# Kernel tuning notes

Hardware: AMD Instinct MI355X
Metric: run time of the kernel (lower is better)

## Reference

```python
import jax, jax.numpy as jnp
import numpy as np

IN_FEATURES = 512
OUT_FEATURES = 512
GRID_MIN = -2.0
GRID_MAX = 2.0
NUM_GRIDS = 8
SPLINE_SCALE = 0.1
BATCH = 16384


def setup_inputs() -> dict:
    key = jax.random.key(0)
    kx, kw = jax.random.split(key)
    x = jax.random.normal(kx, (BATCH, IN_FEATURES), dtype=jnp.float32)
    grid = jnp.linspace(GRID_MIN, GRID_MAX, NUM_GRIDS, dtype=jnp.float32)
    spline_weight = (
        jax.random.normal(kw, (IN_FEATURES * NUM_GRIDS, OUT_FEATURES), dtype=jnp.float32)
        * SPLINE_SCALE
    )
    return {"x": x, "grid": grid, "spline_weight": spline_weight}


def reference(x, grid, spline_weight):
    # denominator h = (grid_max - grid_min) / (num_grids - 1)
    h = (GRID_MAX - GRID_MIN) / (NUM_GRIDS - 1)
    # basis: [B, in_features, num_grids]
    basis = jnp.exp(-jnp.square((x[..., None] - grid) / h))
    # flatten to [B, in_features * num_grids] and GEMM
    return basis.reshape(basis.shape[0], -1) @ spline_weight
```

## Files before the change

### kernel.cpp

```cpp
#include <hip/hip_runtime.h>
#include <hip/hip_bf16.h>

#define BATCH 16384
#define IN_F 512
#define OUT_F 512
#define NG 8
#define KTOT (IN_F * NG)

#define SH    2.1019642153762872f
#define SSTEP 1.2011224087864498f
#define BC0N  4.2039284307525745f
#define RC1   2.4022448175728996f
#define RC2  -1.4426950408889634f
#define RQ    0.13533528323661270f

typedef __attribute__((ext_vector_type(8))) short short8;
typedef __attribute__((ext_vector_type(4))) float f32x4;
typedef __attribute__((ext_vector_type(2))) float f32x2;
typedef __attribute__((ext_vector_type(4))) unsigned int u32x4;
typedef __attribute__((ext_vector_type(2))) unsigned int u32x2;

__device__ __forceinline__ unsigned fbits(float f) {
    union { float f; unsigned u; } v; v.f = f; return v.u;
}
__device__ __forceinline__ unsigned pack2bf(float lo, float hi) {
    unsigned a = (fbits(lo) + 0x8000u) >> 16;
    unsigned b = (fbits(hi) + 0x8000u) & 0xFFFF0000u;
    return a | b;
}

__device__ __forceinline__ void lds_barrier() {
    __asm__ volatile("" ::: "memory");
    __builtin_amdgcn_sched_barrier(0);
    __builtin_amdgcn_s_waitcnt(0xC07F);
    __builtin_amdgcn_s_barrier();
    __builtin_amdgcn_sched_barrier(0);
    __asm__ volatile("" ::: "memory");
}

__global__ void wt_swizzle(const float* __restrict__ W, unsigned short* __restrict__ Wt) {
    const int gid  = blockIdx.x * 256 + threadIdx.x;
    const int lane = gid & 63;
    const int f    = (gid >> 6) & 7;
    const int kt   = (gid >> 9) & 63;
    const int s    = gid >> 15;
    const int j  = f & 3, kk = f >> 2;
    const int l15 = lane & 15, lq = lane >> 4;
    const int n  = s * 64 + j * 16 + l15;
    const int k0 = kt * 64 + kk * 32 + lq * 8;
    u32x4 pk;
#pragma unroll
    for (int e = 0; e < 4; ++e)
        pk[e] = pack2bf(W[(size_t)(k0 + 2 * e) * OUT_F + n],
                        W[(size_t)(k0 + 2 * e + 1) * OUT_F + n]);
    *(u32x4*)(Wt + (size_t)gid * 8) = pk;
}

__global__ __launch_bounds__(256, 2) void gauss_gemm5(
        const float* __restrict__ X, const unsigned short* __restrict__ Wt,
        float* __restrict__ Out) {
    __shared__ __align__(16) unsigned short sA[2 * 64 * 64];

    const int tid  = threadIdx.x;
    const int lane = tid & 63;
    const int wave = tid >> 6;
    const int cb = blockIdx.x & 1;
    const int rb = blockIdx.x >> 1;
    const int m0 = rb * 64;
    const int n0 = cb * 256;
    const int l15 = lane & 15;
    const int lq  = lane >> 4;
    const int s   = cb * 4 + wave;

    const int aw0 = lane * 64 + (((2 * wave)     ^ (lane & 7)) << 3);
    const int aw1 = lane * 64 + (((2 * wave + 1) ^ (lane & 7)) << 3);
    const float* xlp = X + (size_t)(m0 + lane) * IN_F + wave * 2;

    int aofs[2][4];
#pragma unroll
    for (int kk = 0; kk < 2; ++kk)
#pragma unroll
        for (int i = 0; i < 4; ++i)
            aofs[kk][i] = (i * 16 + l15) * 64 + (((kk * 4 + lq) ^ (l15 & 7)) << 3);

    const unsigned short* bptr = Wt + (size_t)s * 262144 + lane * 8;

    f32x4 acc[4][4];
#pragma unroll
    for (int i = 0; i < 4; ++i)
#pragma unroll
        for (int j = 0; j < 4; ++j)
            acc[i][j] = (f32x4){0.f, 0.f, 0.f, 0.f};

    auto stageA = [&](f32x2 xv, int buf) {
        unsigned short* base = sA + buf * 4096;
#pragma unroll
        for (int h = 0; h < 2; ++h) {
            const float t0 = fmaf(h ? xv.y : xv.x, SH, BC0N);
            float r = __builtin_amdgcn_exp2f(fmaf(t0, RC1, RC2));
            const float v0 = __builtin_amdgcn_exp2f(-t0 * t0);
            const float v1 = v0 * r;
            r *= RQ; const float v2 = v1 * r;
            r *= RQ; const float v3 = v2 * r;
            r *= RQ; const float v4 = v3 * r;
            r *= RQ; const float v5 = v4 * r;
            r *= RQ; const float v6 = v5 * r;
            r *= RQ; const float v7 = v6 * r;
            u32x4 pk;
            pk[0] = pack2bf(v0, v1);
            pk[1] = pack2bf(v2, v3);
            pk[2] = pack2bf(v4, v5);
            pk[3] = pack2bf(v6, v7);
            *(u32x4*)(base + (h ? aw1 : aw0)) = pk;
        }
    };

    short8 bfA[8], bfB[8];
    f32x2 xr;

    {
        f32x2 x0 = *(const f32x2*)(xlp);
        stageA(x0, 0);
#pragma unroll
        for (int f = 0; f < 8; ++f)
            bfA[f] = *(const short8*)(bptr + f * 512);
        xr = *(const f32x2*)(xlp + 8);
        lds_barrier();
    }

#define GG_ITER(KT, BUF, BU, BF)                                               \
    {                                                                          \
        const int kn1 = ((KT) + 1 < 63) ? (KT) + 1 : 63;                       \
        const int kn2 = ((KT) + 2 < 63) ? (KT) + 2 : 63;                       \
        short8 af[2][4];                                                       \
        _Pragma("unroll")                                                      \
        for (int kk = 0; kk < 2; ++kk)                                         \
            _Pragma("unroll")                                                  \
            for (int i = 0; i < 4; ++i)                                        \
                af[kk][i] = *(const short8*)(sA + (BUF) * 4096 + aofs[kk][i]); \
        _Pragma("unroll")                                                      \
        for (int f = 0; f < 8; ++f)                                            \
            BF[f] = *(const short8*)(bptr + (size_t)kn1 * 4096 + f * 512);     \
        stageA(xr, (BUF) ^ 1);                                                 \
        xr = *(const f32x2*)(xlp + (size_t)kn2 * 8);                           \
        _Pragma("unroll")                                                      \
        for (int kk = 0; kk < 2; ++kk)                                         \
            _Pragma("unroll")                                                  \
            for (int i = 0; i < 4; ++i)                                        \
                _Pragma("unroll")                                              \
                for (int j = 0; j < 4; ++j)                                    \
                    acc[i][j] = __builtin_amdgcn_mfma_f32_16x16x32_bf16(       \
                        af[kk][i], BU[kk * 4 + j], acc[i][j], 0, 0, 0);        \
        lds_barrier();                                                         \
    }

    for (int kt = 0; kt < 64; kt += 2) {
        GG_ITER(kt,     0, bfA, bfB)
        GG_ITER(kt + 1, 1, bfB, bfA)
    }
#undef GG_ITER

#pragma unroll
    for (int i = 0; i < 4; ++i) {
        const int r0 = m0 + i * 16 + lq * 4;
#pragma unroll
        for (int j = 0; j < 4; ++j) {
            const int c = n0 + wave * 64 + j * 16 + l15;
#pragma unroll
            for (int e = 0; e < 4; ++e)
                Out[(size_t)(r0 + e) * OUT_F + c] = acc[i][j][e];
        }
    }
}

#define BM 128
#define BN 128
#define BK 64
#define LDA 72
#define LDB 72

__global__ __launch_bounds__(256, 2) void gauss_gemm_fb(
        const float* __restrict__ X, const float* __restrict__ W,
        float* __restrict__ Out) {
    __shared__ __align__(16) unsigned short sA[BM * LDA];
    __shared__ __align__(16) unsigned short sB2[BN * LDB];

    const int tid  = threadIdx.x;
    const int lane = tid & 63;
    const int wave = tid >> 6;
    const int rb = blockIdx.x >> 2;
    const int cbx = blockIdx.x & 3;
    const int m0 = rb * BM;
    const int n0 = cbx * BN;
    const int wr = (wave >> 1) * 64;
    const int wc = (wave & 1) * 64;
    const int l15 = lane & 15;
    const int lq  = lane >> 4;

    f32x4 acc[4][4];
#pragma unroll
    for (int i = 0; i < 4; ++i)
#pragma unroll
        for (int j = 0; j < 4; ++j)
            acc[i][j] = (f32x4){0.f, 0.f, 0.f, 0.f};

    const int arow = tid & 127;
    const int axq  = tid >> 7;

    for (int kt = 0; kt < KTOT / BK; ++kt) {
        const int k0  = kt * BK;
        const int xc0 = kt * (BK / NG);

        const f32x4 xv = *(const f32x4*)(X + (size_t)(m0 + arow) * IN_F + xc0 + 4 * axq);
        unsigned short* sArow = sA + arow * LDA + axq * 32;
#pragma unroll
        for (int j = 0; j < 4; ++j) {
            const float xs = xv[j] * SH;
            u32x4 pk;
#pragma unroll
            for (int g = 0; g < 8; g += 2) {
                float t0 = xs + (BC0N - g * SSTEP);
                float t1 = xs + (BC0N - (g + 1) * SSTEP);
                unsigned u0 = fbits(__builtin_amdgcn_exp2f(-t0 * t0)) + 0x8000u;
                unsigned u1 = fbits(__builtin_amdgcn_exp2f(-t1 * t1)) + 0x8000u;
                pk[g >> 1] = (u0 >> 16) | (u1 & 0xFFFF0000u);
            }
            *(u32x4*)(sArow + j * 8) = pk;
        }

#pragma unroll
        for (int p = 0; p < 8; ++p) {
            int id = p * 256 + tid;
            int n  = id & 127;
            int k4 = id >> 7;
            const float* wp = W + (size_t)(k0 + k4 * 4) * OUT_F + n0 + n;
            u32x2 v;
            v[0] = pack2bf(wp[0], wp[OUT_F]);
            v[1] = pack2bf(wp[2 * OUT_F], wp[3 * OUT_F]);
            *(u32x2*)(sB2 + n * LDB + k4 * 4) = v;
        }

        __syncthreads();

#pragma unroll
        for (int kk = 0; kk < BK; kk += 32) {
            short8 af[4], bfv[4];
#pragma unroll
            for (int i = 0; i < 4; ++i)
                af[i] = *(const short8*)(sA + (wr + i * 16 + l15) * LDA + kk + lq * 8);
#pragma unroll
            for (int i = 0; i < 4; ++i)
                bfv[i] = *(const short8*)(sB2 + (wc + i * 16 + l15) * LDB + kk + lq * 8);
#pragma unroll
            for (int i = 0; i < 4; ++i)
#pragma unroll
                for (int j = 0; j < 4; ++j)
                    acc[i][j] = __builtin_amdgcn_mfma_f32_16x16x32_bf16(af[i], bfv[j], acc[i][j], 0, 0, 0);
        }

        __syncthreads();
    }

#pragma unroll
    for (int i = 0; i < 4; ++i) {
        const int r0 = m0 + wr + i * 16 + lq * 4;
#pragma unroll
        for (int j = 0; j < 4; ++j) {
            const int c = n0 + wc + j * 16 + l15;
#pragma unroll
            for (int e = 0; e < 4; ++e)
                Out[(size_t)(r0 + e) * OUT_F + c] = acc[i][j][e];
        }
    }
}

extern "C" void kernel_launch(void* const* d_in, const int* in_sizes, int n_in,
                              void* d_out, int out_size, void* d_ws, size_t ws_size,
                              hipStream_t stream) {
    (void)in_sizes; (void)n_in; (void)out_size;
    const float* X = (const float*)d_in[0];
    const float* W = (const float*)d_in[2];
    float* Out = (float*)d_out;

    const size_t wt_bytes = (size_t)KTOT * OUT_F * sizeof(unsigned short);
    if (ws_size >= wt_bytes) {
        unsigned short* Wt = (unsigned short*)d_ws;
        wt_swizzle<<<dim3(KTOT * OUT_F / 8 / 256), 256, 0, stream>>>(W, Wt);
        gauss_gemm5<<<dim3((BATCH / 64) * (OUT_F / 256)), 256, 0, stream>>>(X, Wt, Out);
    } else {
        gauss_gemm_fb<<<dim3((BATCH / BM) * (OUT_F / BN)), 256, 0, stream>>>(X, W, Out);
    }
}
```

Baseline: 153.7 us.

## Fold Gaussian ratio constants into weights, remap blocks, reorder loads, add priority

Folds the per-grid constant factors exp(-g^2) of the Gaussian recurrence into the weights during the swizzle pass. The in-kernel basis recurrence then multiplies by a single ratio with no per-step rescale. It also uses v_perm for bf16 packing, remaps block indices so the eight blocks dispatched together share column blocks differently, issues the B-fragment global loads before the LDS reads, and raises wave priority around the MFMA chain. Pre-scaling the weights by factors as small as about 1e-22 risks bf16 precision loss in the tail terms.

```diff
diff --git a/kernel.cpp b/kernel.cpp
--- a/kernel.cpp
+++ b/kernel.cpp
@@ -11,8 +11,6 @@
 #define SSTEP 1.2011224087864498f
 #define BC0N  4.2039284307525745f
 #define RC1   2.4022448175728996f
-#define RC2  -1.4426950408889634f
-#define RQ    0.13533528323661270f
 
 typedef __attribute__((ext_vector_type(8))) short short8;
 typedef __attribute__((ext_vector_type(4))) float f32x4;
@@ -24,9 +22,8 @@
     union { float f; unsigned u; } v; v.f = f; return v.u;
 }
 __device__ __forceinline__ unsigned pack2bf(float lo, float hi) {
-    unsigned a = (fbits(lo) + 0x8000u) >> 16;
-    unsigned b = (fbits(hi) + 0x8000u) & 0xFFFF0000u;
-    return a | b;
+    return __builtin_amdgcn_perm(fbits(hi) + 0x8000u, fbits(lo) + 0x8000u,
+                                 0x07060302u);
 }
 
 __device__ __forceinline__ void lds_barrier() {
@@ -48,15 +45,23 @@
     const int l15 = lane & 15, lq = lane >> 4;
     const int n  = s * 64 + j * 16 + l15;
     const int k0 = kt * 64 + kk * 32 + lq * 8;
+    constexpr float QS[8] = {1.0f,
+                             3.6787944117144233e-1f,
+                             1.8315638888734179e-2f,
+                             1.2340980408667956e-4f,
+                             1.1253517471925912e-7f,
+                             1.3887943864964021e-11f,
+                             2.3195228302435693e-16f,
+                             5.2428856633634640e-22f};
     u32x4 pk;
 #pragma unroll
     for (int e = 0; e < 4; ++e)
-        pk[e] = pack2bf(W[(size_t)(k0 + 2 * e) * OUT_F + n],
-                        W[(size_t)(k0 + 2 * e + 1) * OUT_F + n]);
+        pk[e] = pack2bf(W[(size_t)(k0 + 2 * e) * OUT_F + n] * QS[2 * e],
+                        W[(size_t)(k0 + 2 * e + 1) * OUT_F + n] * QS[2 * e + 1]);
     *(u32x4*)(Wt + (size_t)gid * 8) = pk;
 }
 
-__global__ __launch_bounds__(256, 2) void gauss_gemm5(
+__global__ __launch_bounds__(256, 2) void gauss_gemm9(
         const float* __restrict__ X, const unsigned short* __restrict__ Wt,
         float* __restrict__ Out) {
     __shared__ __align__(16) unsigned short sA[2 * 64 * 64];
@@ -64,8 +69,9 @@
     const int tid  = threadIdx.x;
     const int lane = tid & 63;
     const int wave = tid >> 6;
-    const int cb = blockIdx.x & 1;
-    const int rb = blockIdx.x >> 1;
+    const int nb = (blockIdx.x & 7) * 64 + (blockIdx.x >> 3);
+    const int cb = nb >> 8;
+    const int rb = nb & 255;
     const int m0 = rb * 64;
     const int n0 = cb * 256;
     const int l15 = lane & 15;
@@ -96,16 +102,16 @@
         unsigned short* base = sA + buf * 4096;
 #pragma unroll
         for (int h = 0; h < 2; ++h) {
-            const float t0 = fmaf(h ? xv.y : xv.x, SH, BC0N);
-            float r = __builtin_amdgcn_exp2f(fmaf(t0, RC1, RC2));
-            const float v0 = __builtin_amdgcn_exp2f(-t0 * t0);
-            const float v1 = v0 * r;
-            r *= RQ; const float v2 = v1 * r;
-            r *= RQ; const float v3 = v2 * r;
-            r *= RQ; const float v4 = v3 * r;
-            r *= RQ; const float v5 = v4 * r;
-            r *= RQ; const float v6 = v5 * r;
-            r *= RQ; const float v7 = v6 * r;
+            const float t0  = fmaf(h ? xv.y : xv.x, SH, BC0N);
+            const float rho = __builtin_amdgcn_exp2f(t0 * RC1);
+            const float v0  = __builtin_amdgcn_exp2f(-t0 * t0);
+            const float v1 = v0 * rho;
+            const float v2 = v1 * rho;
+            const float v3 = v2 * rho;
+            const float v4 = v3 * rho;
+            const float v5 = v4 * rho;
+            const float v6 = v5 * rho;
+            const float v7 = v6 * rho;
             u32x4 pk;
             pk[0] = pack2bf(v0, v1);
             pk[1] = pack2bf(v2, v3);
@@ -132,17 +138,19 @@
     {                                                                          \
         const int kn1 = ((KT) + 1 < 63) ? (KT) + 1 : 63;                       \
         const int kn2 = ((KT) + 2 < 63) ? (KT) + 2 : 63;                       \
+        _Pragma("unroll")                                                      \
+        for (int f = 0; f < 8; ++f)                                            \
+            BF[f] = *(const short8*)(bptr + (size_t)kn1 * 4096 + f * 512);     \
         short8 af[2][4];                                                       \
         _Pragma("unroll")                                                      \
         for (int kk = 0; kk < 2; ++kk)                                         \
             _Pragma("unroll")                                                  \
             for (int i = 0; i < 4; ++i)                                        \
                 af[kk][i] = *(const short8*)(sA + (BUF) * 4096 + aofs[kk][i]); \
-        _Pragma("unroll")                                                      \
-        for (int f = 0; f < 8; ++f)                                            \
-            BF[f] = *(const short8*)(bptr + (size_t)kn1 * 4096 + f * 512);     \
+        f32x2 xn = *(const f32x2*)(xlp + (size_t)kn2 * 8);                     \
         stageA(xr, (BUF) ^ 1);                                                 \
-        xr = *(const f32x2*)(xlp + (size_t)kn2 * 8);                           \
+        xr = xn;                                                               \
+        __builtin_amdgcn_s_setprio(1);                                         \
         _Pragma("unroll")                                                      \
         for (int kk = 0; kk < 2; ++kk)                                         \
             _Pragma("unroll")                                                  \
@@ -151,6 +159,7 @@
                 for (int j = 0; j < 4; ++j)                                    \
                     acc[i][j] = __builtin_amdgcn_mfma_f32_16x16x32_bf16(       \
                         af[kk][i], BU[kk * 4 + j], acc[i][j], 0, 0, 0);        \
+        __builtin_amdgcn_s_setprio(0);                                         \
         lds_barrier();                                                         \
     }
 
@@ -221,9 +230,8 @@
             for (int g = 0; g < 8; g += 2) {
                 float t0 = xs + (BC0N - g * SSTEP);
                 float t1 = xs + (BC0N - (g + 1) * SSTEP);
-                unsigned u0 = fbits(__builtin_amdgcn_exp2f(-t0 * t0)) + 0x8000u;
-                unsigned u1 = fbits(__builtin_amdgcn_exp2f(-t1 * t1)) + 0x8000u;
-                pk[g >> 1] = (u0 >> 16) | (u1 & 0xFFFF0000u);
+                pk[g >> 1] = pack2bf(__builtin_amdgcn_exp2f(-t0 * t0),
+                                     __builtin_amdgcn_exp2f(-t1 * t1));
             }
             *(u32x4*)(sArow + j * 8) = pk;
         }
@@ -286,7 +294,7 @@
     if (ws_size >= wt_bytes) {
         unsigned short* Wt = (unsigned short*)d_ws;
         wt_swizzle<<<dim3(KTOT * OUT_F / 8 / 256), 256, 0, stream>>>(W, Wt);
-        gauss_gemm5<<<dim3((BATCH / 64) * (OUT_F / 256)), 256, 0, stream>>>(X, Wt, Out);
+        gauss_gemm9<<<dim3((BATCH / 64) * (OUT_F / 256)), 256, 0, stream>>>(X, Wt, Out);
     } else {
         gauss_gemm_fb<<<dim3((BATCH / BM) * (OUT_F / BN)), 256, 0, stream>>>(X, W, Out);
     }
```

After: 150.9 us. Within noise of the previous version (-1.8%).
